# Kernel optimization log

Measured on AMD Instinct MI355X. Metric: run time of the kernel, lower is better.

Reference implementation:

```python
import jax, jax.numpy as jnp
import numpy as np

B, N, D, S, ITERS = 64, 2048, 256, 8, 3
SCALE = D ** -0.5
EPS_LN = 1e-5

def _ln(x, g, b):
    m = jnp.mean(x, axis=-1, keepdims=True)
    v = jnp.var(x, axis=-1, keepdims=True)
    return (x - m) / jnp.sqrt(v + EPS_LN) * g + b

def setup_inputs() -> dict:
    key = jax.random.key(0)
    ks = jax.random.split(key, 20)
    s = D ** -0.5
    f32 = jnp.float32
    return dict(
        x=jax.random.normal(ks[0], (B, N, D), f32),
        noise=jax.random.normal(ks[1], (B, S, D), f32),
        slots_mu=jax.random.normal(ks[2], (1, 1, D), f32),
        slots_sigma=jax.random.normal(ks[3], (1, 1, D), f32),
        Wq=jax.random.normal(ks[4], (D, D), f32) * s, bq=jnp.zeros((D,), f32),
        Wk=jax.random.normal(ks[5], (D, D), f32) * s, bk=jnp.zeros((D,), f32),
        Wv=jax.random.normal(ks[6], (D, D), f32) * s, bv=jnp.zeros((D,), f32),
        W_ih=jax.random.normal(ks[7], (3 * D, D), f32) * s, b_ih=jnp.zeros((3 * D,), f32),
        W_hh=jax.random.normal(ks[8], (3 * D, D), f32) * s, b_hh=jnp.zeros((3 * D,), f32),
        W1=jax.random.normal(ks[9], (D, D), f32) * s, b1=jnp.zeros((D,), f32),
        W2=jax.random.normal(ks[10], (D, D), f32) * s, b2=jnp.zeros((D,), f32),
        g_in=jnp.ones((D,), f32), be_in=jnp.zeros((D,), f32),
        g_sl=jnp.ones((D,), f32), be_sl=jnp.zeros((D,), f32),
        g_ff=jnp.ones((D,), f32), be_ff=jnp.zeros((D,), f32),
    )

def reference(x, noise, slots_mu, slots_sigma, Wq, bq, Wk, bk, Wv, bv,
              W_ih, b_ih, W_hh, b_hh, W1, b1, W2, b2,
              g_in, be_in, g_sl, be_sl, g_ff, be_ff):
    # slot init: mu + softplus(sigma) * noise  -> [B,S,D]
    slots = slots_mu + jax.nn.softplus(slots_sigma) * noise
    xn = _ln(x, g_in, be_in)
    k = xn @ Wk.T + bk  # [B,N,D]
    v = xn @ Wv.T + bv
    for _ in range(ITERS):
        prev = slots
        q = _ln(slots, g_sl, be_sl) @ Wq.T + bq  # [B,S,D]
        logits = jnp.einsum('bsd,bnd->bsn', q, k) * SCALE
        attn = jax.nn.softmax(logits, axis=-1) + 1e-8  # softmax over inputs, as in source
        attn = attn / jnp.sum(attn, axis=-1, keepdims=True)
        updates = jnp.einsum('bsn,bnd->bsd', attn, v)
        # GRUCell(input=updates, hidden=prev); torch gate order r,z,n
        gi = updates @ W_ih.T + b_ih
        gh = prev @ W_hh.T + b_hh
        ir, iz, i_n = jnp.split(gi, 3, axis=-1)
        hr, hz, h_n = jnp.split(gh, 3, axis=-1)
        r = jax.nn.sigmoid(ir + hr)
        z = jax.nn.sigmoid(iz + hz)
        n = jnp.tanh(i_n + r * h_n)
        slots = (1.0 - z) * n + z * prev
        # residual MLP
        h = jax.nn.relu(_ln(slots, g_ff, be_ff) @ W1.T + b1)
        slots = slots + (h @ W2.T + b2)
    return slots
```

## Files before the change

### kernel.cpp

```cpp
#include <hip/hip_runtime.h>
#include <cstddef>


#define BB 64
#define NN 2048
#define DD 256
#define NCH 32
#define CHK 64
#define NITER 3
#define XPITCH 264

typedef unsigned short u16;
typedef unsigned int u32;
typedef _Float16 h2 __attribute__((ext_vector_type(2)));
typedef _Float16 h4 __attribute__((ext_vector_type(4)));

#if defined(__has_builtin)
#if __has_builtin(__builtin_amdgcn_fdot2)
#define HAS_FDOT2 1
#endif
#endif

#ifdef HAS_FDOT2
#define FDOT2(a,b,c) __builtin_amdgcn_fdot2((a),(b),(c),false)
#else
#define FDOT2(a,b,c) fmaf((float)(a).y,(float)(b).y, fmaf((float)(a).x,(float)(b).x,(c)))
#endif

__device__ __forceinline__ h2 u2h2(u32 v){ union{u32 u; h2 h;} c; c.u=v; return c.h; }
__device__ __forceinline__ float u16f(u16 v){ union{u16 u; _Float16 h;} c; c.u=v; return (float)c.h; }

__global__ __launch_bounds__(256) void kA(const float* __restrict__ noise, const float* __restrict__ mu,
                                          const float* __restrict__ sig, float* __restrict__ S,
                                          const float* __restrict__ Wq, const float* __restrict__ Wk,
                                          const float* __restrict__ bq, const float* __restrict__ Wih,
                                          const float* __restrict__ Wv, const float* __restrict__ bv,
                                          const float* __restrict__ bih,
                                          float* __restrict__ Wqk, float* __restrict__ bqk,
                                          float* __restrict__ Wihv, float* __restrict__ bihv){
  __shared__ float col[256];
  const int t = threadIdx.x;
  const int blk = blockIdx.x;
  if(blk < 256){
    col[t] = Wq[t*256 + blk];
    __syncthreads();
    float acc = 0.f;
    #pragma unroll 4
    for(int j=0;j<256;j++) acc += col[j]*Wk[j*256+t];
    Wqk[blk*256+t] = acc * 0.0625f;
  } else if(blk < 1024){
    int c = blk - 256;
    col[t] = Wih[c*256+t];
    __syncthreads();
    float acc = 0.f;
    #pragma unroll 4
    for(int j=0;j<256;j++) acc += col[j]*Wv[j*256+t];
    Wihv[(size_t)c*256+t] = acc;
  } else if(blk < 1536){
    int i = (blk-1024)*256 + t;
    float sg = sig[t];
    float sp = fmaxf(sg, 0.f) + log1pf(expf(-fabsf(sg)));
    S[i] = mu[t] + sp * noise[i];
  } else if(blk == 1536){
    float acc = 0.f;
    for(int j=0;j<256;j++) acc += bq[j]*Wk[j*256+t];
    bqk[t] = acc * 0.0625f;
  } else {
    for(int c=t;c<768;c+=256){
      float acc = 0.f;
      for(int j=0;j<256;j++) acc += Wih[c*256+j]*bv[j];
      bihv[c] = acc + bih[c];
    }
  }
}

__global__ __launch_bounds__(256) void kB(const float* __restrict__ Wihv, const float* __restrict__ Whh,
                                          const float* __restrict__ W1, const float* __restrict__ W2,
                                          float* __restrict__ WihvT, float* __restrict__ WhhT,
                                          float* __restrict__ W1T, float* __restrict__ W2T,
                                          const float* __restrict__ S0, const float* __restrict__ g_sl,
                                          const float* __restrict__ be_sl, const float* __restrict__ Wqk,
                                          const float* __restrict__ bqk, float* __restrict__ Qq){
  __shared__ float tile[64][65];
  __shared__ float lnA[8][256];
  const int blk = blockIdx.x, t = threadIdx.x;
  if(blk < 128){
    const float* src; float* dst; int R, C, tb;
    if(blk < 48){ src=Wihv; dst=WihvT; R=768; C=256; tb=blk; }
    else if(blk < 96){ src=Whh; dst=WhhT; R=768; C=256; tb=blk-48; }
    else if(blk < 112){ src=W1; dst=W1T; R=256; C=256; tb=blk-96; }
    else { src=W2; dst=W2T; R=256; C=256; tb=blk-112; }
    const int tilesC = C/64;
    const int r0 = (tb/tilesC)*64, c0 = (tb%tilesC)*64;
    const int x = t&63, y = t>>6;
    #pragma unroll
    for(int k=0;k<16;k++) tile[y*16+k][x] = src[(size_t)(r0+y*16+k)*C + c0+x];
    __syncthreads();
    #pragma unroll
    for(int k=0;k<16;k++) dst[(size_t)(c0+y*16+k)*R + r0+x] = tile[x][y*16+k];
    return;
  }
  const int w = t>>6, l = t&63;
  const int r0 = (blk-128)*8;
  #pragma unroll
  for(int rr=0; rr<2; rr++){
    int r = w*2 + rr;
    float4 v = *(const float4*)(S0 + (size_t)(r0+r)*256 + l*4);
    float s1 = v.x+v.y+v.z+v.w;
    float s2 = v.x*v.x+v.y*v.y+v.z*v.z+v.w*v.w;
    #pragma unroll
    for(int off=1; off<64; off<<=1){ s1 += __shfl_xor(s1,off); s2 += __shfl_xor(s2,off); }
    float m = s1*(1.f/256.f);
    float var = s2*(1.f/256.f) - m*m;
    float rs = rsqrtf(var + 1e-5f);
    float4 gg = *(const float4*)(g_sl + l*4);
    float4 bb = *(const float4*)(be_sl + l*4);
    float4 o;
    o.x=(v.x-m)*rs*gg.x+bb.x; o.y=(v.y-m)*rs*gg.y+bb.y;
    o.z=(v.z-m)*rs*gg.z+bb.z; o.w=(v.w-m)*rs*gg.w+bb.w;
    *(float4*)(&lnA[r][l*4]) = o;
  }
  __syncthreads();
  const int c4 = l*4;
  float acc[2][4] = {};
  #pragma unroll 2
  for(int k=0;k<256;k++){
    float4 wv = *(const float4*)(Wqk + (size_t)k*256 + c4);
    float a0 = lnA[2*w][k], a1 = lnA[2*w+1][k];
    acc[0][0]+=a0*wv.x; acc[0][1]+=a0*wv.y; acc[0][2]+=a0*wv.z; acc[0][3]+=a0*wv.w;
    acc[1][0]+=a1*wv.x; acc[1][1]+=a1*wv.y; acc[1][2]+=a1*wv.z; acc[1][3]+=a1*wv.w;
  }
  float4 bq4 = *(const float4*)(bqk + c4);
  #pragma unroll
  for(int rr=0; rr<2; rr++){
    float4 o;
    o.x=acc[rr][0]+bq4.x; o.y=acc[rr][1]+bq4.y; o.z=acc[rr][2]+bq4.z; o.w=acc[rr][3]+bq4.w;
    *(float4*)(Qq + (size_t)(r0+2*w+rr)*256 + c4) = o;
  }
}

__device__ __forceinline__ void attn_core(const u16* xs, const h2 (*qs)[128], float (*plT)[64],
                                          float* mS, float* lS,
                                          float* __restrict__ mP, float* __restrict__ lP,
                                          u16* __restrict__ aPh, int b, int c, int t){
  const int w = t>>6, l = t&63;
  float lg = 0.f;
  {
    const u16* xr = xs + (size_t)l*XPITCH;
    #pragma unroll 4
    for(int d8=0; d8<32; ++d8){
      uint4 u = *(const uint4*)(xr + d8*8);
      h2 xa=u2h2(u.x), xb=u2h2(u.y), xc=u2h2(u.z), xd=u2h2(u.w);
      const h2* qp = &qs[w][d8*4];
      lg = FDOT2(xa, qp[0], lg);
      lg = FDOT2(xb, qp[1], lg);
      lg = FDOT2(xc, qp[2], lg);
      lg = FDOT2(xd, qp[3], lg);
    }
  }
  float mx = lg;
  #pragma unroll
  for(int off=1; off<64; off<<=1) mx = fmaxf(mx, __shfl_xor(mx, off));
  float p = __expf(lg - mx);
  float sm = p;
  #pragma unroll
  for(int off=1; off<64; off<<=1) sm += __shfl_xor(sm, off);
  plT[w][l] = p;
  if(l==0){ mS[w] = mx; lS[w] = sm; }
  __syncthreads();
  const size_t pb = (size_t)(b*NCH + c)*8;
  {
    float4 a4 = {0.f,0.f,0.f,0.f};
    const u16* xq = xs + 4*l;
    #pragma unroll 8
    for(int nn=0; nn<64; ++nn){
      uint2 u = *(const uint2*)(xq + (size_t)nn*XPITCH);
      h2 ha=u2h2(u.x), hb=u2h2(u.y);
      float pp = plT[w][nn];
      a4.x += pp*(float)ha.x; a4.y += pp*(float)ha.y;
      a4.z += pp*(float)hb.x; a4.w += pp*(float)hb.y;
    }
    union { h4 h; uint2 u2v; } pk;
    pk.h[0]=(_Float16)a4.x; pk.h[1]=(_Float16)a4.y;
    pk.h[2]=(_Float16)a4.z; pk.h[3]=(_Float16)a4.w;
    *(uint2*)(aPh + (pb + w)*256 + l*4) = pk.u2v;
  }
  if(t<8){ mP[pb+t] = mS[t]; lP[pb+t] = lS[t]; }
}

__global__ __launch_bounds__(512) void k_attn0(const float* __restrict__ x, const float* __restrict__ g_in,
                                               const float* __restrict__ be_in, u16* __restrict__ xn,
                                               const float* __restrict__ Qq,
                                               float* __restrict__ mP, float* __restrict__ lP,
                                               u16* __restrict__ aPh){
  __shared__ __align__(16) u16 xs[CHK*XPITCH];
  __shared__ h2 qs[8][128];
  __shared__ float plT[8][64];
  __shared__ float mS[8], lS[8];
  const int b = blockIdx.x, c = blockIdx.y, t = threadIdx.x;
  const int w = t>>6, l = t&63;
  {
    const size_t rowbase = (size_t)b*NN + (size_t)c*CHK;
    const float* xb = x + rowbase*DD;
    float4 gg = *(const float4*)(g_in + l*4);
    float4 bb = *(const float4*)(be_in + l*4);
    #pragma unroll
    for(int k=0;k<4;k++){
      int r0 = w + 16*k, r1 = w + 16*k + 8;
      float4 v0 = *(const float4*)(xb + (size_t)r0*256 + l*4);
      float4 v1 = *(const float4*)(xb + (size_t)r1*256 + l*4);
      float a1 = v0.x+v0.y+v0.z+v0.w;
      float a2 = v0.x*v0.x + v0.y*v0.y + v0.z*v0.z + v0.w*v0.w;
      float b1 = v1.x+v1.y+v1.z+v1.w;
      float b2 = v1.x*v1.x + v1.y*v1.y + v1.z*v1.z + v1.w*v1.w;
      #pragma unroll
      for(int off=1; off<64; off<<=1){
        a1 += __shfl_xor(a1,off); a2 += __shfl_xor(a2,off);
        b1 += __shfl_xor(b1,off); b2 += __shfl_xor(b2,off);
      }
      float m0 = a1*(1.f/256.f), va0 = a2*(1.f/256.f) - m0*m0, rs0 = rsqrtf(va0 + 1e-5f);
      float m1 = b1*(1.f/256.f), va1 = b2*(1.f/256.f) - m1*m1, rs1 = rsqrtf(va1 + 1e-5f);
      union { h4 h; uint2 u2v; } p0, p1;
      p0.h[0]=(_Float16)((v0.x-m0)*rs0*gg.x+bb.x); p0.h[1]=(_Float16)((v0.y-m0)*rs0*gg.y+bb.y);
      p0.h[2]=(_Float16)((v0.z-m0)*rs0*gg.z+bb.z); p0.h[3]=(_Float16)((v0.w-m0)*rs0*gg.w+bb.w);
      p1.h[0]=(_Float16)((v1.x-m1)*rs1*gg.x+bb.x); p1.h[1]=(_Float16)((v1.y-m1)*rs1*gg.y+bb.y);
      p1.h[2]=(_Float16)((v1.z-m1)*rs1*gg.z+bb.z); p1.h[3]=(_Float16)((v1.w-m1)*rs1*gg.w+bb.w);
      *(uint2*)(xs + (size_t)r0*XPITCH + l*4) = p0.u2v;
      *(uint2*)(xs + (size_t)r1*XPITCH + l*4) = p1.u2v;
      *(uint2*)(xn + (rowbase+r0)*DD + l*4) = p0.u2v;
      *(uint2*)(xn + (rowbase+r1)*DD + l*4) = p1.u2v;
    }
  }
  for(int i=t; i<1024; i+=512){
    int s = i>>7, p = i&127;
    float a = Qq[b*2048 + s*256 + 2*p];
    float bq = Qq[b*2048 + s*256 + 2*p + 1];
    h2 hv; hv.x = (_Float16)a; hv.y = (_Float16)bq;
    qs[s][p] = hv;
  }
  __syncthreads();
  attn_core(xs, qs, plT, mS, lS, mP, lP, aPh, b, c, t);
}

__global__ __launch_bounds__(512) void k_attnN(const u16* __restrict__ xn, const float* __restrict__ Qq,
                                               float* __restrict__ mP, float* __restrict__ lP,
                                               u16* __restrict__ aPh){
  __shared__ __align__(16) u16 xs[CHK*XPITCH];
  __shared__ h2 qs[8][128];
  __shared__ float plT[8][64];
  __shared__ float mS[8], lS[8];
  const int b = blockIdx.x, c = blockIdx.y, t = threadIdx.x;
  {
    const uint4* xg4 = (const uint4*)(xn + ((size_t)b*NN + (size_t)c*CHK)*DD);
    #pragma unroll
    for(int k=0;k<4;k++){
      int idx = t + 512*k;
      int n = idx>>5, j = idx&31;
      *(uint4*)(xs + (size_t)n*XPITCH + j*8) = xg4[idx];
    }
  }
  for(int i=t; i<1024; i+=512){
    int s = i>>7, p = i&127;
    float a = Qq[b*2048 + s*256 + 2*p];
    float bq = Qq[b*2048 + s*256 + 2*p + 1];
    h2 hv; hv.x = (_Float16)a; hv.y = (_Float16)bq;
    qs[s][p] = hv;
  }
  __syncthreads();
  attn_core(xs, qs, plT, mS, lS, mP, lP, aPh, b, c, t);
}

union PostU {
  float Gt[2][4][768];
  struct { float Row[4][256]; float Ht[4][256]; float Lq[4][256]; } m;
};

__global__ __launch_bounds__(512) void k_post(const float* __restrict__ mP, const float* __restrict__ lP,
                                              const u16* __restrict__ aPh, const float* __restrict__ WihvT,
                                              const float* __restrict__ bihv, const float* __restrict__ WhhT,
                                              const float* __restrict__ bhh, const float* __restrict__ Sc,
                                              const float* __restrict__ g_ff, const float* __restrict__ be_ff,
                                              const float* __restrict__ W1T, const float* __restrict__ b1,
                                              const float* __restrict__ W2T, const float* __restrict__ b2,
                                              const float* __restrict__ g_sl, const float* __restrict__ be_sl,
                                              const float* __restrict__ Wqk, const float* __restrict__ bqk,
                                              float* __restrict__ Sout, float* __restrict__ Qq, int writeQ){
  __shared__ float Ut[4][256];
  __shared__ float Sp[4][256];
  __shared__ float Hp[2][4][256];
  __shared__ PostU uu;
  __shared__ float red2[4][2];
  const int t = threadIdx.x;
  const int r0 = blockIdx.x*4;
  const int b = r0>>3;
  const int w = t>>6, l = t&63;
  const int c = t&255, hh = t>>8;

  #pragma unroll
  for(int k=0;k<2;k++){
    int idx = t + 512*k;
    int r = idx>>8, cc = idx&255;
    int rr = r0 + r, ss = rr&7;
    const float* mpb = mP + b*(NCH*8) + ss;
    const float* lpb = lP + b*(NCH*8) + ss;
    float M = -1e30f;
    #pragma unroll
    for(int c8=0;c8<NCH;c8++) M = fmaxf(M, mpb[c8*8]);
    float L = 0.f;
    float wc[NCH];
    #pragma unroll
    for(int c8=0;c8<NCH;c8++){ wc[c8] = __expf(mpb[c8*8] - M); L += lpb[c8*8]*wc[c8]; }
    float inv = 1.f/L;
    size_t base = ((size_t)b*(NCH*8) + ss)*256 + cc;
    float u = 0.f;
    #pragma unroll
    for(int c8=0;c8<NCH;c8++) u += wc[c8]*u16f(aPh[base + (size_t)c8*2048]);
    Ut[r][cc] = u*inv;
    Sp[r][cc] = Sc[(size_t)rr*256 + cc];
  }
  __syncthreads();

  if(t < 384){
    const int mat = t/192, q4 = (t - mat*192)*4;
    const float* WT = mat ? WhhT : WihvT;
    const float* bb2 = mat ? bhh : bihv;
    const float (*A)[256] = mat ? Sp : Ut;
    float4 bias4 = *(const float4*)(bb2 + q4);
    float4 ac0 = bias4, ac1 = bias4, ac2 = bias4, ac3 = bias4;
    const float* wp = WT + q4;
    #pragma unroll 4
    for(int d=0; d<256; ++d){
      float4 wv = *(const float4*)(wp + (size_t)d*768);
      float a0=A[0][d], a1=A[1][d], a2=A[2][d], a3=A[3][d];
      ac0.x += a0*wv.x; ac0.y += a0*wv.y; ac0.z += a0*wv.z; ac0.w += a0*wv.w;
      ac1.x += a1*wv.x; ac1.y += a1*wv.y; ac1.z += a1*wv.z; ac1.w += a1*wv.w;
      ac2.x += a2*wv.x; ac2.y += a2*wv.y; ac2.z += a2*wv.z; ac2.w += a2*wv.w;
      ac3.x += a3*wv.x; ac3.y += a3*wv.y; ac3.z += a3*wv.z; ac3.w += a3*wv.w;
    }
    *(float4*)(&uu.Gt[mat][0][q4]) = ac0;
    *(float4*)(&uu.Gt[mat][1][q4]) = ac1;
    *(float4*)(&uu.Gt[mat][2][q4]) = ac2;
    *(float4*)(&uu.Gt[mat][3][q4]) = ac3;
  }
  __syncthreads();

  #pragma unroll
  for(int k=0;k<2;k++){
    int idx = t + 512*k;
    int r = idx>>8, cc = idx&255;
    float gir = uu.Gt[0][r][cc], giz = uu.Gt[0][r][256+cc], gin = uu.Gt[0][r][512+cc];
    float ghr = uu.Gt[1][r][cc], ghz = uu.Gt[1][r][256+cc], ghn = uu.Gt[1][r][512+cc];
    float rr2 = 1.f/(1.f + __expf(-(gir+ghr)));
    float zz = 1.f/(1.f + __expf(-(giz+ghz)));
    float nn = tanhf(gin + rr2*ghn);
    Ut[r][cc] = (1.f-zz)*nn + zz*Sp[r][cc];
  }
  __syncthreads();

  if(w < 4){
    float s1=0.f, s2=0.f;
    #pragma unroll
    for(int k2=0;k2<4;k2++){ float v = Ut[w][l + 64*k2]; s1 += v; s2 += v*v; }
    #pragma unroll
    for(int off=1; off<64; off<<=1){ s1 += __shfl_xor(s1,off); s2 += __shfl_xor(s2,off); }
    if(l==0){
      float m = s1*(1.f/256.f);
      float var = s2*(1.f/256.f) - m*m;
      red2[w][0] = m; red2[w][1] = rsqrtf(var + 1e-5f);
    }
  }
  __syncthreads();
  #pragma unroll
  for(int k=0;k<2;k++){
    int idx = t + 512*k;
    int r = idx>>8, cc = idx&255;
    uu.m.Row[r][cc] = (Ut[r][cc]-red2[r][0])*red2[r][1]*g_ff[cc] + be_ff[cc];
  }
  __syncthreads();

  {
    const float* w1 = W1T + (size_t)hh*128*256 + c;
    float a0 = hh ? 0.f : b1[c], a1=a0, a2=a0, a3=a0;
    const int dB = hh*128;
    #pragma unroll 8
    for(int d=0; d<128; ++d){
      float wv = w1[(size_t)d*256];
      a0 += uu.m.Row[0][dB+d]*wv;
      a1 += uu.m.Row[1][dB+d]*wv;
      a2 += uu.m.Row[2][dB+d]*wv;
      a3 += uu.m.Row[3][dB+d]*wv;
    }
    Hp[hh][0][c]=a0; Hp[hh][1][c]=a1; Hp[hh][2][c]=a2; Hp[hh][3][c]=a3;
  }
  __syncthreads();
  #pragma unroll
  for(int k=0;k<2;k++){
    int idx = t + 512*k;
    int r = idx>>8, cc = idx&255;
    uu.m.Ht[r][cc] = fmaxf(Hp[0][r][cc]+Hp[1][r][cc], 0.f);
  }
  __syncthreads();

  {
    const float* w2 = W2T + (size_t)hh*128*256 + c;
    float a0 = hh ? 0.f : b2[c], a1=a0, a2=a0, a3=a0;
    const int dB = hh*128;
    #pragma unroll 8
    for(int d=0; d<128; ++d){
      float wv = w2[(size_t)d*256];
      a0 += uu.m.Ht[0][dB+d]*wv;
      a1 += uu.m.Ht[1][dB+d]*wv;
      a2 += uu.m.Ht[2][dB+d]*wv;
      a3 += uu.m.Ht[3][dB+d]*wv;
    }
    Hp[hh][0][c]=a0; Hp[hh][1][c]=a1; Hp[hh][2][c]=a2; Hp[hh][3][c]=a3;
  }
  __syncthreads();
  if(t < 256){
    #pragma unroll
    for(int r=0;r<4;r++){
      float sn = Hp[0][r][c] + Hp[1][r][c] + Ut[r][c];
      Sout[(size_t)(r0+r)*256 + c] = sn;
      Ut[r][c] = sn;
    }
  }

  if(writeQ){
    __syncthreads();
    if(w < 4){
      float s1=0.f, s2=0.f;
      #pragma unroll
      for(int k2=0;k2<4;k2++){ float v = Ut[w][l + 64*k2]; s1 += v; s2 += v*v; }
      #pragma unroll
      for(int off=1; off<64; off<<=1){ s1 += __shfl_xor(s1,off); s2 += __shfl_xor(s2,off); }
      if(l==0){
        float m = s1*(1.f/256.f);
        float var = s2*(1.f/256.f) - m*m;
        red2[w][0] = m; red2[w][1] = rsqrtf(var + 1e-5f);
      }
    }
    __syncthreads();
    #pragma unroll
    for(int k=0;k<2;k++){
      int idx = t + 512*k;
      int r = idx>>8, cc = idx&255;
      uu.m.Lq[r][cc] = (Ut[r][cc]-red2[r][0])*red2[r][1]*g_sl[cc] + be_sl[cc];
    }
    __syncthreads();
    {
      const float* wq = Wqk + (size_t)hh*128*256 + c;
      float a0 = hh ? 0.f : bqk[c], a1=a0, a2=a0, a3=a0;
      const int dB = hh*128;
      #pragma unroll 8
      for(int d=0; d<128; ++d){
        float wv = wq[(size_t)d*256];
        a0 += uu.m.Lq[0][dB+d]*wv;
        a1 += uu.m.Lq[1][dB+d]*wv;
        a2 += uu.m.Lq[2][dB+d]*wv;
        a3 += uu.m.Lq[3][dB+d]*wv;
      }
      Hp[hh][0][c]=a0; Hp[hh][1][c]=a1; Hp[hh][2][c]=a2; Hp[hh][3][c]=a3;
    }
    __syncthreads();
    if(t < 256){
      #pragma unroll
      for(int r=0;r<4;r++)
        Qq[(size_t)(r0+r)*256 + c] = Hp[0][r][c] + Hp[1][r][c];
    }
  }
}

extern "C" void kernel_launch(void* const* d_in, const int* in_sizes, int n_in,
                              void* d_out, int out_size, void* d_ws, size_t ws_size,
                              hipStream_t stream){
  const float* x    = (const float*)d_in[0];
  const float* noise= (const float*)d_in[1];
  const float* mu   = (const float*)d_in[2];
  const float* sig  = (const float*)d_in[3];
  const float* Wq   = (const float*)d_in[4];
  const float* bq   = (const float*)d_in[5];
  const float* Wk   = (const float*)d_in[6];
  const float* Wv   = (const float*)d_in[8];
  const float* bv   = (const float*)d_in[9];
  const float* W_ih = (const float*)d_in[10];
  const float* b_ih = (const float*)d_in[11];
  const float* W_hh = (const float*)d_in[12];
  const float* b_hh = (const float*)d_in[13];
  const float* W1m  = (const float*)d_in[14];
  const float* b1v  = (const float*)d_in[15];
  const float* W2m  = (const float*)d_in[16];
  const float* b2v  = (const float*)d_in[17];
  const float* g_in = (const float*)d_in[18];
  const float* be_in= (const float*)d_in[19];
  const float* g_sl = (const float*)d_in[20];
  const float* be_sl= (const float*)d_in[21];
  const float* g_ff = (const float*)d_in[22];
  const float* be_ff= (const float*)d_in[23];

  char* p = (char*)d_ws;
  auto alloc = [&](size_t bytes)->char*{ char* q = p; p += (bytes + 255) & ~(size_t)255; return q; };
  u16*   xn    = (u16*)  alloc((size_t)BB*NN*DD*2);
  float* Wqk   = (float*)alloc(256*256*4);
  float* bqk   = (float*)alloc(256*4);
  float* Wihv  = (float*)alloc((size_t)768*256*4);
  float* WihvT = (float*)alloc((size_t)256*768*4);
  float* bihv  = (float*)alloc(768*4);
  float* WhhT  = (float*)alloc((size_t)256*768*4);
  float* W1T   = (float*)alloc(256*256*4);
  float* W2T   = (float*)alloc(256*256*4);
  float* S0    = (float*)alloc(512*256*4);
  float* S1    = (float*)alloc(512*256*4);
  float* Qq    = (float*)alloc(512*256*4);
  float* mP    = (float*)alloc(64*NCH*8*4);
  float* lP    = (float*)alloc(64*NCH*8*4);
  u16*   aPh   = (u16*)  alloc((size_t)64*NCH*8*256*2);
  if((size_t)(p - (char*)d_ws) > ws_size) return;

  kA<<<1538, 256, 0, stream>>>(noise, mu, sig, S0, Wq, Wk, bq, W_ih, Wv, bv, b_ih,
                               Wqk, bqk, Wihv, bihv);
  kB<<<192, 256, 0, stream>>>(Wihv, W_hh, W1m, W2m, WihvT, WhhT, W1T, W2T,
                              S0, g_sl, be_sl, Wqk, bqk, Qq);

  float* Sin = S0;
  float* Sping[2] = { S1, S0 };
  for(int it=0; it<NITER; ++it){
    float* Sout = (it==NITER-1) ? (float*)d_out : Sping[it&1];
    if(it == 0)
      k_attn0<<<dim3(64, NCH), 512, 0, stream>>>(x, g_in, be_in, xn, Qq, mP, lP, aPh);
    else
      k_attnN<<<dim3(64, NCH), 512, 0, stream>>>(xn, Qq, mP, lP, aPh);
    k_post<<<128, 512, 0, stream>>>(mP, lP, aPh, WihvT, bihv, WhhT, b_hh, Sin, g_ff, be_ff,
                                    W1T, b1v, W2T, b2v, g_sl, be_sl, Wqk, bqk,
                                    Sout, Qq, (it<NITER-1) ? 1 : 0);
    Sin = Sout;
  }
}
```

Measured before the change: 311.9 us.

## Make attention blocks persistent over four chunks with register prefetch of next chunk

The attention kernels are merged into one templated kernel launched with 512 blocks instead of 2048. Each block processes four chunks of the same batch, and the global loads for the next chunk go into registers while the current chunk's logits, softmax and weighted sum are computed. This aims to hide global-memory latency and amortize the per-block Q staging and launch cost. The trade-off is more registers and one extra barrier per chunk, plus fewer blocks to spread across the GPU's compute units.

Result: slower. 343.9 us (+10.2%).

```diff
diff --git a/kernel.cpp b/kernel.cpp
--- a/kernel.cpp
+++ b/kernel.cpp
@@ -139,56 +139,8 @@
   }
 }
 
-__device__ __forceinline__ void attn_core(const u16* xs, const h2 (*qs)[128], float (*plT)[64],
-                                          float* mS, float* lS,
-                                          float* __restrict__ mP, float* __restrict__ lP,
-                                          u16* __restrict__ aPh, int b, int c, int t){
-  const int w = t>>6, l = t&63;
-  float lg = 0.f;
-  {
-    const u16* xr = xs + (size_t)l*XPITCH;
-    #pragma unroll 4
-    for(int d8=0; d8<32; ++d8){
-      uint4 u = *(const uint4*)(xr + d8*8);
-      h2 xa=u2h2(u.x), xb=u2h2(u.y), xc=u2h2(u.z), xd=u2h2(u.w);
-      const h2* qp = &qs[w][d8*4];
-      lg = FDOT2(xa, qp[0], lg);
-      lg = FDOT2(xb, qp[1], lg);
-      lg = FDOT2(xc, qp[2], lg);
-      lg = FDOT2(xd, qp[3], lg);
-    }
-  }
-  float mx = lg;
-  #pragma unroll
-  for(int off=1; off<64; off<<=1) mx = fmaxf(mx, __shfl_xor(mx, off));
-  float p = __expf(lg - mx);
-  float sm = p;
-  #pragma unroll
-  for(int off=1; off<64; off<<=1) sm += __shfl_xor(sm, off);
-  plT[w][l] = p;
-  if(l==0){ mS[w] = mx; lS[w] = sm; }
-  __syncthreads();
-  const size_t pb = (size_t)(b*NCH + c)*8;
-  {
-    float4 a4 = {0.f,0.f,0.f,0.f};
-    const u16* xq = xs + 4*l;
-    #pragma unroll 8
-    for(int nn=0; nn<64; ++nn){
-      uint2 u = *(const uint2*)(xq + (size_t)nn*XPITCH);
-      h2 ha=u2h2(u.x), hb=u2h2(u.y);
-      float pp = plT[w][nn];
-      a4.x += pp*(float)ha.x; a4.y += pp*(float)ha.y;
-      a4.z += pp*(float)hb.x; a4.w += pp*(float)hb.y;
-    }
-    union { h4 h; uint2 u2v; } pk;
-    pk.h[0]=(_Float16)a4.x; pk.h[1]=(_Float16)a4.y;
-    pk.h[2]=(_Float16)a4.z; pk.h[3]=(_Float16)a4.w;
-    *(uint2*)(aPh + (pb + w)*256 + l*4) = pk.u2v;
-  }
-  if(t<8){ mP[pb+t] = mS[t]; lP[pb+t] = lS[t]; }
-}
-
-__global__ __launch_bounds__(512) void k_attn0(const float* __restrict__ x, const float* __restrict__ g_in,
+template<int ITER0>
+__global__ __launch_bounds__(512) void k_attnP(const float* __restrict__ x, const float* __restrict__ g_in,
                                                const float* __restrict__ be_in, u16* __restrict__ xn,
                                                const float* __restrict__ Qq,
                                                float* __restrict__ mP, float* __restrict__ lP,
@@ -197,77 +149,131 @@
   __shared__ h2 qs[8][128];
   __shared__ float plT[8][64];
   __shared__ float mS[8], lS[8];
-  const int b = blockIdx.x, c = blockIdx.y, t = threadIdx.x;
+  const int g = blockIdx.x, t = threadIdx.x;
+  const int b = g & 63, c0 = g >> 6;
   const int w = t>>6, l = t&63;
-  {
-    const size_t rowbase = (size_t)b*NN + (size_t)c*CHK;
-    const float* xb = x + rowbase*DD;
-    float4 gg = *(const float4*)(g_in + l*4);
-    float4 bb = *(const float4*)(be_in + l*4);
-    #pragma unroll
-    for(int k=0;k<4;k++){
-      int r0 = w + 16*k, r1 = w + 16*k + 8;
-      float4 v0 = *(const float4*)(xb + (size_t)r0*256 + l*4);
-      float4 v1 = *(const float4*)(xb + (size_t)r1*256 + l*4);
-      float a1 = v0.x+v0.y+v0.z+v0.w;
-      float a2 = v0.x*v0.x + v0.y*v0.y + v0.z*v0.z + v0.w*v0.w;
-      float b1 = v1.x+v1.y+v1.z+v1.w;
-      float b2 = v1.x*v1.x + v1.y*v1.y + v1.z*v1.z + v1.w*v1.w;
-      #pragma unroll
-      for(int off=1; off<64; off<<=1){
-        a1 += __shfl_xor(a1,off); a2 += __shfl_xor(a2,off);
-        b1 += __shfl_xor(b1,off); b2 += __shfl_xor(b2,off);
-      }
-      float m0 = a1*(1.f/256.f), va0 = a2*(1.f/256.f) - m0*m0, rs0 = rsqrtf(va0 + 1e-5f);
-      float m1 = b1*(1.f/256.f), va1 = b2*(1.f/256.f) - m1*m1, rs1 = rsqrtf(va1 + 1e-5f);
-      union { h4 h; uint2 u2v; } p0, p1;
-      p0.h[0]=(_Float16)((v0.x-m0)*rs0*gg.x+bb.x); p0.h[1]=(_Float16)((v0.y-m0)*rs0*gg.y+bb.y);
-      p0.h[2]=(_Float16)((v0.z-m0)*rs0*gg.z+bb.z); p0.h[3]=(_Float16)((v0.w-m0)*rs0*gg.w+bb.w);
-      p1.h[0]=(_Float16)((v1.x-m1)*rs1*gg.x+bb.x); p1.h[1]=(_Float16)((v1.y-m1)*rs1*gg.y+bb.y);
-      p1.h[2]=(_Float16)((v1.z-m1)*rs1*gg.z+bb.z); p1.h[3]=(_Float16)((v1.w-m1)*rs1*gg.w+bb.w);
-      *(uint2*)(xs + (size_t)r0*XPITCH + l*4) = p0.u2v;
-      *(uint2*)(xs + (size_t)r1*XPITCH + l*4) = p1.u2v;
-      *(uint2*)(xn + (rowbase+r0)*DD + l*4) = p0.u2v;
-      *(uint2*)(xn + (rowbase+r1)*DD + l*4) = p1.u2v;
-    }
-  }
+
   for(int i=t; i<1024; i+=512){
     int s = i>>7, p = i&127;
-    float a = Qq[b*2048 + s*256 + 2*p];
-    float bq = Qq[b*2048 + s*256 + 2*p + 1];
-    h2 hv; hv.x = (_Float16)a; hv.y = (_Float16)bq;
+    h2 hv;
+    hv.x = (_Float16)Qq[b*2048 + s*256 + 2*p];
+    hv.y = (_Float16)Qq[b*2048 + s*256 + 2*p + 1];
     qs[s][p] = hv;
   }
-  __syncthreads();
-  attn_core(xs, qs, plT, mS, lS, mP, lP, aPh, b, c, t);
-}
-
-__global__ __launch_bounds__(512) void k_attnN(const u16* __restrict__ xn, const float* __restrict__ Qq,
-                                               float* __restrict__ mP, float* __restrict__ lP,
-                                               u16* __restrict__ aPh){
-  __shared__ __align__(16) u16 xs[CHK*XPITCH];
-  __shared__ h2 qs[8][128];
-  __shared__ float plT[8][64];
-  __shared__ float mS[8], lS[8];
-  const int b = blockIdx.x, c = blockIdx.y, t = threadIdx.x;
+  float4 gg, bb;
+  if(ITER0){ gg = *(const float4*)(g_in + l*4); bb = *(const float4*)(be_in + l*4); }
+
+  float4 pf[ITER0 ? 8 : 4];
+
   {
-    const uint4* xg4 = (const uint4*)(xn + ((size_t)b*NN + (size_t)c*CHK)*DD);
-    #pragma unroll
-    for(int k=0;k<4;k++){
-      int idx = t + 512*k;
-      int n = idx>>5, j = idx&31;
-      *(uint4*)(xs + (size_t)n*XPITCH + j*8) = xg4[idx];
-    }
-  }
-  for(int i=t; i<1024; i+=512){
-    int s = i>>7, p = i&127;
-    float a = Qq[b*2048 + s*256 + 2*p];
-    float bq = Qq[b*2048 + s*256 + 2*p + 1];
-    h2 hv; hv.x = (_Float16)a; hv.y = (_Float16)bq;
-    qs[s][p] = hv;
-  }
-  __syncthreads();
-  attn_core(xs, qs, plT, mS, lS, mP, lP, aPh, b, c, t);
+    const int c = c0;
+    if(ITER0){
+      const float* xb = x + ((size_t)b*NN + (size_t)c*CHK)*DD;
+      #pragma unroll
+      for(int j=0;j<8;j++)
+        pf[j] = *(const float4*)(xb + (size_t)(w+8*j)*256 + l*4);
+    } else {
+      const uint4* xg4 = (const uint4*)(xn + ((size_t)b*NN + (size_t)c*CHK)*DD);
+      #pragma unroll
+      for(int k=0;k<4;k++)
+        *(uint4*)&pf[k] = xg4[t + 512*k];
+    }
+  }
+
+  #pragma unroll
+  for(int i=0;i<4;i++){
+    const int c = c0 + 8*i;
+    if(ITER0){
+      const size_t rowbase = (size_t)b*NN + (size_t)c*CHK;
+      #pragma unroll
+      for(int j=0;j<8;j++){
+        int row = w + 8*j;
+        float4 v = pf[j];
+        float s1 = v.x+v.y+v.z+v.w;
+        float s2 = v.x*v.x + v.y*v.y + v.z*v.z + v.w*v.w;
+        #pragma unroll
+        for(int off=1; off<64; off<<=1){ s1 += __shfl_xor(s1,off); s2 += __shfl_xor(s2,off); }
+        float m = s1*(1.f/256.f);
+        float var = s2*(1.f/256.f) - m*m;
+        float rs = rsqrtf(var + 1e-5f);
+        union { h4 h; uint2 u2v; } pk;
+        pk.h[0] = (_Float16)((v.x-m)*rs*gg.x + bb.x);
+        pk.h[1] = (_Float16)((v.y-m)*rs*gg.y + bb.y);
+        pk.h[2] = (_Float16)((v.z-m)*rs*gg.z + bb.z);
+        pk.h[3] = (_Float16)((v.w-m)*rs*gg.w + bb.w);
+        *(uint2*)(xs + (size_t)row*XPITCH + l*4) = pk.u2v;
+        *(uint2*)(xn + (rowbase+row)*DD + l*4) = pk.u2v;
+      }
+    } else {
+      #pragma unroll
+      for(int k=0;k<4;k++){
+        int idx = t + 512*k;
+        int n = idx>>5, j = idx&31;
+        *(uint4*)(xs + (size_t)n*XPITCH + j*8) = *(uint4*)&pf[k];
+      }
+    }
+    __syncthreads();
+
+    if(i < 3){
+      const int cn = c0 + 8*(i+1);
+      if(ITER0){
+        const float* xb = x + ((size_t)b*NN + (size_t)cn*CHK)*DD;
+        #pragma unroll
+        for(int j=0;j<8;j++)
+          pf[j] = *(const float4*)(xb + (size_t)(w+8*j)*256 + l*4);
+      } else {
+        const uint4* xg4 = (const uint4*)(xn + ((size_t)b*NN + (size_t)cn*CHK)*DD);
+        #pragma unroll
+        for(int k=0;k<4;k++)
+          *(uint4*)&pf[k] = xg4[t + 512*k];
+      }
+    }
+
+    float lg = 0.f;
+    {
+      const u16* xr = xs + (size_t)l*XPITCH;
+      #pragma unroll 4
+      for(int d8=0; d8<32; ++d8){
+        uint4 u = *(const uint4*)(xr + d8*8);
+        h2 xa=u2h2(u.x), xb2=u2h2(u.y), xc=u2h2(u.z), xd=u2h2(u.w);
+        const h2* qp = &qs[w][d8*4];
+        lg = FDOT2(xa, qp[0], lg);
+        lg = FDOT2(xb2, qp[1], lg);
+        lg = FDOT2(xc, qp[2], lg);
+        lg = FDOT2(xd, qp[3], lg);
+      }
+    }
+    float mx = lg;
+    #pragma unroll
+    for(int off=1; off<64; off<<=1) mx = fmaxf(mx, __shfl_xor(mx, off));
+    float p = __expf(lg - mx);
+    float sm = p;
+    #pragma unroll
+    for(int off=1; off<64; off<<=1) sm += __shfl_xor(sm, off);
+    plT[w][l] = p;
+    if(l==0){ mS[w] = mx; lS[w] = sm; }
+    __syncthreads();
+
+    const size_t pb = (size_t)(b*NCH + c)*8;
+    {
+      float4 a4 = {0.f,0.f,0.f,0.f};
+      const u16* xq = xs + 4*l;
+      #pragma unroll 8
+      for(int nn=0; nn<64; ++nn){
+        uint2 u = *(const uint2*)(xq + (size_t)nn*XPITCH);
+        h2 ha=u2h2(u.x), hb=u2h2(u.y);
+        float pp = plT[w][nn];
+        a4.x += pp*(float)ha.x; a4.y += pp*(float)ha.y;
+        a4.z += pp*(float)hb.x; a4.w += pp*(float)hb.y;
+      }
+      union { h4 h; uint2 u2v; } pk;
+      pk.h[0]=(_Float16)a4.x; pk.h[1]=(_Float16)a4.y;
+      pk.h[2]=(_Float16)a4.z; pk.h[3]=(_Float16)a4.w;
+      *(uint2*)(aPh + (pb + w)*256 + l*4) = pk.u2v;
+    }
+    if(t<8){ mP[pb+t] = mS[t]; lP[pb+t] = lS[t]; }
+    __syncthreads();
+  }
 }
 
 union PostU {
@@ -526,9 +532,9 @@
   for(int it=0; it<NITER; ++it){
     float* Sout = (it==NITER-1) ? (float*)d_out : Sping[it&1];
     if(it == 0)
-      k_attn0<<<dim3(64, NCH), 512, 0, stream>>>(x, g_in, be_in, xn, Qq, mP, lP, aPh);
+      k_attnP<1><<<512, 512, 0, stream>>>(x, g_in, be_in, xn, Qq, mP, lP, aPh);
     else
-      k_attnN<<<dim3(64, NCH), 512, 0, stream>>>(xn, Qq, mP, lP, aPh);
+      k_attnP<0><<<512, 512, 0, stream>>>(x, g_in, be_in, xn, Qq, mP, lP, aPh);
     k_post<<<128, 512, 0, stream>>>(mP, lP, aPh, WihvT, bihv, WhhT, b_hh, Sin, g_ff, be_ff,
                                     W1T, b1v, W2T, b2v, g_sl, be_sl, Wqk, bqk,
                                     Sout, Qq, (it<NITER-1) ? 1 : 0);
```
